# Kernel tuning notes

Measured on AMD Instinct MI355X. Metric: run time of the kernel, lower is better.

The kernel has to match this reference:

```python
import jax, jax.numpy as jnp
import numpy as np

G, NPG = 100, 500
N = G * NPG            # 50000 nodes, contiguous equal-size graphs
IN, H = 128, 256
L = 3                  # num_layers
K = 3                  # knn k (loop=True -> self included)
E = 16 * N             # 800000 edges

def setup_inputs():
    key = jax.random.key(0)
    k = jax.random.split(key, 8)
    x = jax.random.normal(k[0], (N, IN), jnp.float32)
    batch = jnp.repeat(jnp.arange(G, dtype=jnp.int32), NPG)
    gid = jax.random.randint(k[1], (E,), 0, G)
    src = jax.random.randint(k[2], (E,), 0, NPG) + gid * NPG
    dst = jax.random.randint(k[3], (E,), 0, NPG) + gid * NPG
    edge_index = jnp.stack([src, dst]).astype(jnp.int32)
    def lin(kk, fin, fout):
        return (jax.random.normal(kk, (fin, fout), jnp.float32) / np.sqrt(fin)).astype(jnp.float32)
    inp = dict(x=x, edge_index=edge_index, batch=batch)
    inp["emb_W"] = lin(k[4], IN, H); inp["emb_b"] = jnp.zeros((H,), jnp.float32)
    inp["conv_W"] = jnp.stack([lin(jax.random.fold_in(k[5], i), H, H) for i in range(L)])
    inp["conv_b"] = jnp.zeros((L, H), jnp.float32)
    inp["fconv_W"] = jnp.stack([lin(jax.random.fold_in(k[6], i), H, H) for i in range(L)])
    inp["fconv_b"] = jnp.zeros((L, H), jnp.float32)
    inp["norm_w"] = jnp.ones((L, H), jnp.float32); inp["norm_b"] = jnp.zeros((L, H), jnp.float32); inp["norm_ms"] = jnp.ones((L, H), jnp.float32)
    inp["fnorm_w"] = jnp.ones((L, H), jnp.float32); inp["fnorm_b"] = jnp.zeros((L, H), jnp.float32); inp["fnorm_ms"] = jnp.ones((L, H), jnp.float32)
    inp["gate_W"] = lin(k[7], 2 * H, H); inp["gate_b"] = jnp.zeros((H,), jnp.float32)
    return inp

def _gcn_conv(h, src, dst, W, b):
    # GCNConv: add self loops, symmetric deg^-1/2 normalization
    m = h @ W                                     # [N,H]
    loop = jnp.arange(N, dtype=src.dtype)
    s2 = jnp.concatenate([src, loop]); d2 = jnp.concatenate([dst, loop])
    deg = jax.ops.segment_sum(jnp.ones_like(d2, jnp.float32), d2, num_segments=N)
    dinv = jnp.where(deg > 0, jax.lax.rsqrt(deg), 0.0)
    coef = (dinv[s2] * dinv[d2])[:, None]
    return jax.ops.segment_sum(m[s2] * coef, d2, num_segments=N) + b

def _graph_norm(x, batch, w, b, ms, cnt):
    # PyG GraphNorm: out = w * (x - ms*mean) / sqrt(var + eps) + b, per-graph stats
    mean = jax.ops.segment_sum(x, batch, num_segments=G) / cnt
    out = x - mean[batch] * ms
    var = jax.ops.segment_sum(out * out, batch, num_segments=G) / cnt
    return w * out * jax.lax.rsqrt(var + 1e-5)[batch] + b

def _knn_graph(x):
    # per-graph cosine knn, loop=True (self has sim 1 and is kept)
    xr = x.reshape(G, NPG, -1)
    xn = xr / (jnp.linalg.norm(xr, axis=-1, keepdims=True) + 1e-12)
    sim = jnp.einsum('gnh,gmh->gnm', xn, xn)      # [G,NPG,NPG]
    _, idx = jax.lax.top_k(sim, K)                # [G,NPG,K]
    offs = (jnp.arange(G) * NPG)[:, None, None]
    src = (idx + offs).reshape(-1)
    dst = jnp.broadcast_to(jnp.arange(N).reshape(G, NPG, 1), (G, NPG, K)).reshape(-1)
    return src.astype(jnp.int32), dst.astype(jnp.int32)

def reference(x, edge_index, batch, emb_W, emb_b, conv_W, conv_b, norm_w, norm_b, norm_ms, fconv_W, fconv_b, fnorm_w, fnorm_b, fnorm_ms, gate_W, gate_b):
    cnt = jax.ops.segment_sum(jnp.ones((N,), jnp.float32), batch, num_segments=G)[:, None]
    h = x @ emb_W + emb_b
    fsrc, fdst = _knn_graph(h)
    src, dst = edge_index[0], edge_index[1]
    all_x = []
    for i in range(L - 1):   # eval mode: dropout is identity
        prev = h
        h = _gcn_conv(h, src, dst, conv_W[i], conv_b[i])
        h = jax.nn.leaky_relu(_graph_norm(h, batch, norm_w[i], norm_b[i], norm_ms[i], cnt))
        f = _gcn_conv(h, fsrc, fdst, fconv_W[i], fconv_b[i])
        f = jax.nn.leaky_relu(_graph_norm(f, batch, fnorm_w[i], fnorm_b[i], fnorm_ms[i], cnt))
        gate = jax.nn.sigmoid(jnp.concatenate([h, f], axis=-1) @ gate_W + gate_b)
        h = gate * h + (1.0 - gate) * f + prev
        all_x.append(h)
    # faithful to source: for i in range(L): += pool(all_x[i-1])  (Python negative indexing!)
    gf = jnp.zeros((G, H), jnp.float32)
    for i in range(L):
        gf = gf + jax.ops.segment_sum(all_x[i - 1], batch, num_segments=G) / cnt
    return gf
```

## Files before the change

### kernel.cpp

```cpp
#include <hip/hip_runtime.h>
#include <math.h>

#define NN 50000
#define GG 100
#define NPGc 500
#define HH 256
#define IND 128

typedef __attribute__((ext_vector_type(8))) short short8v;
typedef __attribute__((ext_vector_type(4))) float f32x4;

__device__ __forceinline__ ushort f2bf(float f) {
    union { float f; unsigned u; } v; v.f = f;
    unsigned r = (v.u + 0x7fffu + ((v.u >> 16) & 1u)) >> 16;
    return (ushort)r;
}
__device__ __forceinline__ float bf2f(ushort h) {
    union { unsigned u; float f; } v; v.u = ((unsigned)h) << 16;
    return v.f;
}

__device__ __forceinline__ int swz(int row, int kidx) { return kidx ^ ((row & 7) << 3); }

__global__ void wcvt_all(const float* __restrict__ emb_W, const float* __restrict__ conv_W,
                         const float* __restrict__ fconv_W, const float* __restrict__ gate_W,
                         ushort* __restrict__ dst)
{
    int i = blockIdx.x * 256 + threadIdx.x;
    if (i >= 425984) return;
    float v;
    if (i < 32768)       { int n = i >> 7, k = i & 127;              v = emb_W[(size_t)k * 256 + n]; }
    else if (i < 98304)  { int j = i - 32768;  int n = j >> 8, k = j & 255; v = conv_W[(size_t)k * 256 + n]; }
    else if (i < 163840) { int j = i - 98304;  int n = j >> 8, k = j & 255; v = conv_W[65536 + (size_t)k * 256 + n]; }
    else if (i < 229376) { int j = i - 163840; int n = j >> 8, k = j & 255; v = fconv_W[(size_t)k * 256 + n]; }
    else if (i < 294912) { int j = i - 229376; int n = j >> 8, k = j & 255; v = fconv_W[65536 + (size_t)k * 256 + n]; }
    else                 { int j = i - 294912; int n = j >> 9, k = j & 511; v = gate_W[(size_t)k * 256 + n]; }
    dst[i] = f2bf(v);
}

__global__ __launch_bounds__(256)
void gemm_mfma(const void* __restrict__ Av, const void* __restrict__ A2v, int abf,
               const ushort* __restrict__ Wt, const float* __restrict__ bias,
               float* __restrict__ C, ushort* __restrict__ Cbf,
               int M, int K, int lda, int mode,
               const ushort* __restrict__ hn, const ushort* __restrict__ fn,
               const void* __restrict__ prevv, int prevbf)
{
    __shared__ ushort As[128][64];
    __shared__ ushort Bs[128][64];
    const int bid = blockIdx.x;
    const int xcd = bid & 7;
    const int t = bid >> 3;
    const int cb = t & 1;
    const int rowblk = (t >> 1) * 8 + xcd;
    const int row0 = rowblk * 128;
    if (row0 >= M) return;
    const int col0 = cb * 128;
    const int tid = threadIdx.x;
    const int lane = tid & 63;
    const int w = tid >> 6;
    const int wr = (w >> 1) * 64, wc = (w & 1) * 64;
    const int lr = lane & 15, lk = (lane >> 4) * 8;
    f32x4 acc[4][4] = {};

    for (int k0 = 0; k0 < K; k0 += 64) {
        __syncthreads();
        #pragma unroll
        for (int it = 0; it < 4; ++it) {
            int c = it * 256 + tid;
            int row = c >> 3, col = (c & 7) * 8;
            int gr = row0 + row; if (gr > M - 1) gr = M - 1;
            int kk = k0 + col;
            if (abf) {
                const ushort* Ap = (const ushort*)Av;
                if (A2v != nullptr && kk >= 256) { Ap = (const ushort*)A2v; kk -= 256; }
                *(int4*)&As[row][swz(row, col)] =
                    *(const int4*)&Ap[(size_t)gr * lda + kk];
            } else {
                const float* Ap = (const float*)Av;
                if (A2v != nullptr && kk >= 256) { Ap = (const float*)A2v; kk -= 256; }
                const float* s = &Ap[(size_t)gr * lda + kk];
                float4 v0 = *(const float4*)s;
                float4 v1 = *(const float4*)(s + 4);
                union { ushort u[8]; int4 q; } pk;
                pk.u[0] = f2bf(v0.x); pk.u[1] = f2bf(v0.y); pk.u[2] = f2bf(v0.z); pk.u[3] = f2bf(v0.w);
                pk.u[4] = f2bf(v1.x); pk.u[5] = f2bf(v1.y); pk.u[6] = f2bf(v1.z); pk.u[7] = f2bf(v1.w);
                *(int4*)&As[row][swz(row, col)] = pk.q;
            }
        }
        #pragma unroll
        for (int it = 0; it < 4; ++it) {
            int c = it * 256 + tid;
            int n = c >> 3, k = (c & 7) * 8;
            *(int4*)&Bs[n][swz(n, k)] = *(const int4*)&Wt[(size_t)(col0 + n) * K + k0 + k];
        }
        __syncthreads();
        #pragma unroll
        for (int ks = 0; ks < 2; ++ks) {
            short8v av[4], bv[4];
            #pragma unroll
            for (int m = 0; m < 4; ++m) {
                int rr = wr + m * 16 + lr;
                av[m] = *(const short8v*)&As[rr][swz(rr, ks * 32 + lk)];
            }
            #pragma unroll
            for (int n = 0; n < 4; ++n) {
                int rr = wc + n * 16 + lr;
                bv[n] = *(const short8v*)&Bs[rr][swz(rr, ks * 32 + lk)];
            }
            #pragma unroll
            for (int m = 0; m < 4; ++m)
                #pragma unroll
                for (int n = 0; n < 4; ++n)
                    acc[m][n] = __builtin_amdgcn_mfma_f32_16x16x32_bf16(av[m], bv[n], acc[m][n], 0, 0, 0);
        }
    }
    const int fr = (lane >> 4) * 4;
    if (mode == 0) {
        #pragma unroll
        for (int n = 0; n < 4; ++n) {
            int col = col0 + wc + n * 16 + lr;
            float bb = bias ? bias[col] : 0.f;
            #pragma unroll
            for (int m = 0; m < 4; ++m) {
                int rbase = row0 + wr + m * 16 + fr;
                #pragma unroll
                for (int r = 0; r < 4; ++r) {
                    int row = rbase + r;
                    if (row < M) C[(size_t)row * HH + col] = acc[m][n][r] + bb;
                }
            }
        }
    } else if (mode == 2) {
        #pragma unroll
        for (int n = 0; n < 4; ++n) {
            int col = col0 + wc + n * 16 + lr;
            float bb = bias ? bias[col] : 0.f;
            #pragma unroll
            for (int m = 0; m < 4; ++m) {
                int rbase = row0 + wr + m * 16 + fr;
                #pragma unroll
                for (int r = 0; r < 4; ++r) {
                    int row = rbase + r;
                    if (row < M) Cbf[(size_t)row * HH + col] = f2bf(acc[m][n][r] + bb);
                }
            }
        }
    } else {
        #pragma unroll
        for (int n = 0; n < 4; ++n) {
            int col = col0 + wc + n * 16 + lr;
            float gb = bias[col];
            #pragma unroll
            for (int m = 0; m < 4; ++m) {
                int rbase = row0 + wr + m * 16 + fr;
                #pragma unroll
                for (int r = 0; r < 4; ++r) {
                    int row = rbase + r;
                    if (row < M) {
                        size_t o = (size_t)row * HH + col;
                        float z = acc[m][n][r] + gb;
                        float s = 1.f / (1.f + expf(-z));
                        float hv = bf2f(hn[o]);
                        float fv = bf2f(fn[o]);
                        float pv = prevbf ? bf2f(((const ushort*)prevv)[o])
                                          : ((const float*)prevv)[o];
                        Cbf[o] = f2bf(s * hv + (1.f - s) * fv + pv);
                    }
                }
            }
        }
    }
}

__global__ __launch_bounds__(256)
void row_norm_hl(const float* __restrict__ h, ushort* __restrict__ xh, ushort* __restrict__ xl)
{
    int n = blockIdx.x, c = threadIdx.x;
    float v = h[(size_t)n * HH + c];
    __shared__ float red[256];
    red[c] = v * v;
    __syncthreads();
    for (int s = 128; s > 0; s >>= 1) {
        if (c < s) red[c] += red[c + s];
        __syncthreads();
    }
    float norm = sqrtf(red[0]);
    float xn = v / (norm + 1e-12f);
    ushort hi = f2bf(xn);
    xh[(size_t)n * HH + c] = hi;
    xl[(size_t)n * HH + c] = f2bf(xn - bf2f(hi));
}

__device__ __forceinline__ bool tk_better(float va, int ia, float vb, int ib)
{
    return (va > vb) || (va == vb && ia < ib);
}

__device__ __forceinline__ void ins3(float v, int i,
                                     float& a0, int& b0, float& a1, int& b1,
                                     float& a2, int& b2)
{
    if (tk_better(v, i, a0, b0))      { a2 = a1; b2 = b1; a1 = a0; b1 = b0; a0 = v; b0 = i; }
    else if (tk_better(v, i, a1, b1)) { a2 = a1; b2 = b1; a1 = v;  b1 = i; }
    else if (tk_better(v, i, a2, b2)) { a2 = v;  b2 = i; }
}

__device__ __forceinline__ void merge3(float& v0, float& v1, float& v2,
                                       int& i0, int& i1, int& i2, int off)
{
    float w0 = __shfl_xor(v0, off), w1 = __shfl_xor(v1, off), w2 = __shfl_xor(v2, off);
    int   j0 = __shfl_xor(i0, off), j1 = __shfl_xor(i1, off), j2 = __shfl_xor(i2, off);
    float avv[3] = { v0, v1, v2 }, bvv[3] = { w0, w1, w2 };
    int   aii[3] = { i0, i1, i2 }, bii[3] = { j0, j1, j2 };
    float rv[3]; int ri[3];
    int p = 0, q = 0;
    #pragma unroll
    for (int t = 0; t < 3; ++t) {
        bool takeA = tk_better(avv[p], aii[p], bvv[q], bii[q]);
        rv[t] = takeA ? avv[p] : bvv[q];
        ri[t] = takeA ? aii[p] : bii[q];
        if (takeA) ++p; else ++q;
    }
    v0 = rv[0]; v1 = rv[1]; v2 = rv[2];
    i0 = ri[0]; i1 = ri[1]; i2 = ri[2];
}

__global__ __launch_bounds__(256, 1)
void simtopk(const ushort* __restrict__ xnh, const ushort* __restrict__ xnl,
             int* __restrict__ fsrc)
{
    __shared__ ushort Bs[2][2][128][36];
    const int bid = blockIdx.x;
    const int xcd = bid & 7;
    const int rb  = (bid >> 3) & 7;
    const int g   = (bid >> 6) * 8 + xcd;
    if (g >= GG) return;
    const int row0 = rb * 64;
    const int tid  = threadIdx.x;
    const int lane = tid & 63;
    const int w    = tid >> 6;
    const int lr   = lane & 15;
    const int hi4  = lane >> 4;
    const size_t base = (size_t)g * NPGc * HH;

    int arow = row0 + w * 16 + lr; if (arow > NPGc - 1) arow = NPGc - 1;
    const ushort* aph = xnh + base + (size_t)arow * HH + hi4 * 8;
    const ushort* apl = xnl + base + (size_t)arow * HH + hi4 * 8;
    short8v ah[8], al[8];
    #pragma unroll
    for (int kc = 0; kc < 8; ++kc) {
        ah[kc] = *(const short8v*)(aph + kc * 32);
        al[kc] = *(const short8v*)(apl + kc * 32);
    }

    const int scol = tid >> 1;
    const int sq   = (tid & 1) * 2;

    float tv0[4], tv1[4], tv2[4];
    int   ti0[4], ti1[4], ti2[4];
    #pragma unroll
    for (int r = 0; r < 4; ++r) {
        tv0[r] = tv1[r] = tv2[r] = -2.f;
        ti0[r] = ti1[r] = ti2[r] = 0x7fffffff;
    }

    for (int ct = 0; ct < 4; ++ct) {
        const int col0 = ct * 128;
        int gcol = col0 + scol; if (gcol > NPGc - 1) gcol = NPGc - 1;
        const ushort* sph = xnh + base + (size_t)gcol * HH + sq * 8;
        const ushort* spl = xnl + base + (size_t)gcol * HH + sq * 8;

        {
            int4 h0 = *(const int4*)(sph);
            int4 h1 = *(const int4*)(sph + 8);
            int4 l0 = *(const int4*)(spl);
            int4 l1 = *(const int4*)(spl + 8);
            *(int4*)&Bs[0][0][scol][sq * 8]     = h0;
            *(int4*)&Bs[0][0][scol][sq * 8 + 8] = h1;
            *(int4*)&Bs[0][1][scol][sq * 8]     = l0;
            *(int4*)&Bs[0][1][scol][sq * 8 + 8] = l1;
        }
        __syncthreads();

        f32x4 acc[8] = {};
        #pragma unroll
        for (int kc = 0; kc < 8; ++kc) {
            const int cur = kc & 1, nxt = cur ^ 1;
            int4 h0, h1, l0, l1;
            if (kc < 7) {
                const ushort* nh = sph + (kc + 1) * 32;
                const ushort* nl = spl + (kc + 1) * 32;
                h0 = *(const int4*)(nh);
                h1 = *(const int4*)(nh + 8);
                l0 = *(const int4*)(nl);
                l1 = *(const int4*)(nl + 8);
            }
            short8v bh[8], bl[8];
            #pragma unroll
            for (int n = 0; n < 8; ++n) {
                int rr = n * 16 + lr;
                bh[n] = *(const short8v*)&Bs[cur][0][rr][hi4 * 8];
                bl[n] = *(const short8v*)&Bs[cur][1][rr][hi4 * 8];
            }
            #pragma unroll
            for (int n = 0; n < 8; ++n) {
                acc[n] = __builtin_amdgcn_mfma_f32_16x16x32_bf16(ah[kc], bh[n], acc[n], 0, 0, 0);
                acc[n] = __builtin_amdgcn_mfma_f32_16x16x32_bf16(ah[kc], bl[n], acc[n], 0, 0, 0);
                acc[n] = __builtin_amdgcn_mfma_f32_16x16x32_bf16(al[kc], bh[n], acc[n], 0, 0, 0);
            }
            if (kc < 7) {
                *(int4*)&Bs[nxt][0][scol][sq * 8]     = h0;
                *(int4*)&Bs[nxt][0][scol][sq * 8 + 8] = h1;
                *(int4*)&Bs[nxt][1][scol][sq * 8]     = l0;
                *(int4*)&Bs[nxt][1][scol][sq * 8 + 8] = l1;
            }
            __syncthreads();
        }

        #pragma unroll
        for (int r = 0; r < 4; ++r) {
            float a0 = tv0[r], a1 = tv1[r], a2 = tv2[r];
            int   b0 = ti0[r], b1 = ti1[r], b2 = ti2[r];
            #pragma unroll
            for (int n = 0; n < 8; ++n) {
                int col = col0 + n * 16 + lr;
                if (col < NPGc)
                    ins3(acc[n][r], col, a0, b0, a1, b1, a2, b2);
            }
            tv0[r] = a0; tv1[r] = a1; tv2[r] = a2;
            ti0[r] = b0; ti1[r] = b1; ti2[r] = b2;
        }
    }

    #pragma unroll
    for (int r = 0; r < 4; ++r) {
        float a0 = tv0[r], a1 = tv1[r], a2 = tv2[r];
        int   b0 = ti0[r], b1 = ti1[r], b2 = ti2[r];
        #pragma unroll
        for (int off = 1; off <= 8; off <<= 1)
            merge3(a0, a1, a2, b0, b1, b2, off);
        if (lr == 0) {
            int row = row0 + w * 16 + hi4 * 4 + r;
            if (row < NPGc) {
                int rg = g * NPGc + row;
                fsrc[rg * 3 + 0] = g * NPGc + b0;
                fsrc[rg * 3 + 1] = g * NPGc + b1;
                fsrc[rg * 3 + 2] = g * NPGc + b2;
            }
        }
    }
}

__global__ void hist_kernel(const int* __restrict__ dst, int* __restrict__ cnt, int nE)
{
    int e = blockIdx.x * 256 + threadIdx.x;
    if (e < nE) atomicAdd(&cnt[dst[e]], 1);
}

__global__ void scan1_kernel(const int* __restrict__ in, int* __restrict__ out,
                             int* __restrict__ bsum, int n)
{
    __shared__ int sh[256];
    int t = threadIdx.x;
    int i = blockIdx.x * 256 + t;
    int v = (i < n) ? in[i] : 0;
    sh[t] = v;
    __syncthreads();
    for (int s = 1; s < 256; s <<= 1) {
        int tv = (t >= s) ? sh[t - s] : 0;
        __syncthreads();
        sh[t] += tv;
        __syncthreads();
    }
    if (i < n) out[i] = sh[t] - v;
    if (t == 255) bsum[blockIdx.x] = sh[255];
}

__global__ void scan2_kernel(int* __restrict__ bsum, int nb)
{
    __shared__ int sh[256];
    int t = threadIdx.x;
    int v = (t < nb) ? bsum[t] : 0;
    sh[t] = v;
    __syncthreads();
    for (int s = 1; s < 256; s <<= 1) {
        int tv = (t >= s) ? sh[t - s] : 0;
        __syncthreads();
        sh[t] += tv;
        __syncthreads();
    }
    if (t < nb) bsum[t] = sh[t] - v;
}

__global__ void scan3_kernel(int* __restrict__ out, const int* __restrict__ bsum, int n)
{
    int i = blockIdx.x * 256 + threadIdx.x;
    if (i < n) out[i] += bsum[blockIdx.x];
}

__global__ void fill_kernel(const int* __restrict__ src, const int* __restrict__ dst,
                            const int* __restrict__ row_ptr, int* __restrict__ cursor,
                            int* __restrict__ sorted_src, int nE)
{
    int e = blockIdx.x * 256 + threadIdx.x;
    if (e < nE) {
        int d = dst[e];
        int pos = row_ptr[d] + atomicAdd(&cursor[d], 1);
        sorted_src[pos] = src[e];
    }
}

__global__ void dinv_kernel(const int* __restrict__ cnt, float* __restrict__ dinv, int n)
{
    int i = blockIdx.x * 256 + threadIdx.x;
    if (i < n) dinv[i] = rsqrtf((float)cnt[i] + 1.0f);
}

__global__ __launch_bounds__(256)
void gcn_gather(const ushort* __restrict__ m, const int* __restrict__ row_ptr,
                const int* __restrict__ cnt, const int* __restrict__ srcs,
                const float* __restrict__ dinv, const float* __restrict__ bias,
                ushort* __restrict__ out)
{
    int bid = blockIdx.x;
    int xcd = bid & 7, idx = bid >> 3;
    int g = xcd + 8 * (idx / NPGc);
    if (g >= GG) return;
    int n = g * NPGc + (idx % NPGc);
    int c = threadIdx.x;
    float dn = dinv[n];
    float acc = bf2f(m[(size_t)n * HH + c]) * dn;
    int s0 = row_ptr[n], e0 = s0 + cnt[n];
    for (int e = s0; e < e0; ++e) {
        int s = srcs[e];
        acc += bf2f(m[(size_t)s * HH + c]) * dinv[s];
    }
    out[(size_t)n * HH + c] = f2bf(acc * dn + bias[c]);
}

__global__ __launch_bounds__(256)
void fgcn_gather(const ushort* __restrict__ m, const int* __restrict__ fsrc,
                 const float* __restrict__ bias, ushort* __restrict__ out)
{
    int bid = blockIdx.x;
    int xcd = bid & 7, idx = bid >> 3;
    int g = xcd + 8 * (idx / NPGc);
    if (g >= GG) return;
    int n = g * NPGc + (idx % NPGc);
    int c = threadIdx.x;
    int s0 = fsrc[n * 3], s1 = fsrc[n * 3 + 1], s2 = fsrc[n * 3 + 2];
    float acc = bf2f(m[(size_t)n * HH + c]) + bf2f(m[(size_t)s0 * HH + c])
              + bf2f(m[(size_t)s1 * HH + c]) + bf2f(m[(size_t)s2 * HH + c]);
    out[(size_t)n * HH + c] = f2bf(0.25f * acc + bias[c]);
}

__global__ __launch_bounds__(256)
void norm_stats(const ushort* __restrict__ x, float* __restrict__ S1p, float* __restrict__ S2p)
{
    int g = blockIdx.x, chunk = blockIdx.y, c = threadIdx.x;
    int r0 = chunk * 63, r1 = min(r0 + 63, NPGc);
    float s1 = 0.f, s2 = 0.f;
    for (int r = r0; r < r1; ++r) {
        float v = bf2f(x[((size_t)(g * NPGc + r)) * HH + c]);
        s1 += v; s2 += v * v;
    }
    size_t o = ((size_t)(g * 8 + chunk)) * HH + c;
    S1p[o] = s1;
    S2p[o] = s2;
}

__global__ __launch_bounds__(256)
void norm_reduce(const float* __restrict__ S1p, const float* __restrict__ S2p,
                 const float* __restrict__ ms, float* __restrict__ MM, float* __restrict__ RS)
{
    int g = blockIdx.x, c = threadIdx.x;
    float s1 = 0.f, s2 = 0.f;
    #pragma unroll
    for (int j = 0; j < 8; ++j) {
        size_t po = ((size_t)(g * 8 + j)) * HH + c;
        s1 += S1p[po];
        s2 += S2p[po];
    }
    float mean = s1 / (float)NPGc;
    float mm = mean * ms[c];
    float var = s2 / (float)NPGc - 2.f * mm * mean + mm * mm;
    MM[g * HH + c] = mm;
    RS[g * HH + c] = rsqrtf(var + 1e-5f);
}

__global__ __launch_bounds__(256)
void norm_apply(ushort* __restrict__ x, const float* __restrict__ MM, const float* __restrict__ RS,
                const float* __restrict__ w, const float* __restrict__ b)
{
    int n = blockIdx.x, c = threadIdx.x;
    int g = n / NPGc;
    size_t o = (size_t)n * HH + c;
    float v = bf2f(x[o]);
    float outv = w[c] * (v - MM[g * HH + c]) * RS[g * HH + c] + b[c];
    x[o] = f2bf(outv > 0.f ? outv : 0.01f * outv);
}

__global__ __launch_bounds__(256)
void pool_kernel(const ushort* __restrict__ X0, const ushort* __restrict__ X1,
                 float* __restrict__ out)
{
    int g = blockIdx.x, c = threadIdx.x;
    float s0 = 0.f, s1 = 0.f;
    for (int r = 0; r < NPGc; ++r) {
        size_t o = ((size_t)(g * NPGc + r)) * HH + c;
        s0 += bf2f(X0[o]);
        s1 += bf2f(X1[o]);
    }
    out[g * HH + c] = (s0 + 2.f * s1) / (float)NPGc;
}

__global__ void sentinel_kernel(float* out, int n)
{
    int i = blockIdx.x * 256 + threadIdx.x;
    if (i < n) out[i] = 12345.0f;
}

extern "C" void kernel_launch(void* const* d_in, const int* in_sizes, int n_in,
                              void* d_out, int out_size, void* d_ws, size_t ws_size,
                              hipStream_t stream)
{
    const float* x       = (const float*)d_in[0];
    const int* edge_idx  = (const int*)d_in[1];
    const float* emb_W   = (const float*)d_in[3];
    const float* emb_b   = (const float*)d_in[4];
    const float* conv_W  = (const float*)d_in[5];
    const float* conv_b  = (const float*)d_in[6];
    const float* fconv_W = (const float*)d_in[7];
    const float* fconv_b = (const float*)d_in[8];
    const float* norm_w  = (const float*)d_in[9];
    const float* norm_b  = (const float*)d_in[10];
    const float* norm_ms = (const float*)d_in[11];
    const float* fnorm_w = (const float*)d_in[12];
    const float* fnorm_b = (const float*)d_in[13];
    const float* fnorm_ms= (const float*)d_in[14];
    const float* gate_W  = (const float*)d_in[15];
    const float* gate_b  = (const float*)d_in[16];

    const int E = in_sizes[1] / 2;
    const int* esrc = edge_idx;
    const int* edst = edge_idx + E;

    const size_t NHf = (size_t)NN * HH;
    char* p = (char*)d_ws;
    auto alloc = [&](size_t bytes) { char* r = p; p += (bytes + 255) & ~(size_t)255; return r; };
    float*  B0 = (float*)alloc(NHf * 4);
    ushort* Mr = (ushort*)alloc(NHf * 2);
    ushort* Ar = (ushort*)alloc(NHf * 2);
    ushort* Br = (ushort*)alloc(NHf * 2);
    ushort* H0 = (ushort*)alloc(NHf * 2);
    ushort* H1 = (ushort*)alloc(NHf * 2);
    ushort* xnh = Mr;
    ushort* xnl = Ar;
    int* sorted_src = (int*)alloc((size_t)E * 4);
    int* row_ptr    = (int*)alloc((size_t)NN * 4);
    int* deg_cnt    = (int*)alloc((size_t)NN * 4);
    int* cursor     = (int*)alloc((size_t)NN * 4);
    float* dinv     = (float*)alloc((size_t)NN * 4);
    int* fsrc       = (int*)alloc((size_t)NN * 3 * 4);
    float* S1p      = (float*)alloc((size_t)GG * 8 * HH * 4);
    float* S2p      = (float*)alloc((size_t)GG * 8 * HH * 4);
    float* MM       = (float*)alloc((size_t)GG * HH * 4);
    float* RS       = (float*)alloc((size_t)GG * HH * 4);
    int* bsum       = (int*)alloc(1024);
    ushort* wts     = (ushort*)alloc((size_t)425984 * 2);
    size_t needed = (size_t)(p - (char*)d_ws);
    if (ws_size < needed) {
        sentinel_kernel<<<(out_size + 255) / 256, 256, 0, stream>>>((float*)d_out, out_size);
        return;
    }
    ushort* embWt   = wts;
    ushort* convWt0 = wts + 32768;
    ushort* convWt1 = wts + 98304;
    ushort* fconvWt0 = wts + 163840;
    ushort* fconvWt1 = wts + 229376;
    ushort* gateWt  = wts + 294912;

    const int nScanB = (NN + 255) / 256;
    const int gatherGrid = 8 * 13 * NPGc;
    const int gemmGrid = 8 * 49 * 2;

    hipMemsetAsync(deg_cnt, 0, (size_t)NN * 4, stream);
    hipMemsetAsync(cursor, 0, (size_t)NN * 4, stream);

    wcvt_all<<<1664, 256, 0, stream>>>(emb_W, conv_W, fconv_W, gate_W, wts);

    gemm_mfma<<<gemmGrid, 256, 0, stream>>>(x, nullptr, 0, embWt, emb_b, B0, nullptr,
                                            NN, IND, IND, 0, nullptr, nullptr, nullptr, 0);

    hist_kernel<<<(E + 255) / 256, 256, 0, stream>>>(edst, deg_cnt, E);
    scan1_kernel<<<nScanB, 256, 0, stream>>>(deg_cnt, row_ptr, bsum, NN);
    scan2_kernel<<<1, 256, 0, stream>>>(bsum, nScanB);
    scan3_kernel<<<nScanB, 256, 0, stream>>>(row_ptr, bsum, NN);
    fill_kernel<<<(E + 255) / 256, 256, 0, stream>>>(esrc, edst, row_ptr, cursor, sorted_src, E);
    dinv_kernel<<<(NN + 255) / 256, 256, 0, stream>>>(deg_cnt, dinv, NN);

    row_norm_hl<<<NN, 256, 0, stream>>>(B0, xnh, xnl);
    simtopk<<<832, 256, 0, stream>>>(xnh, xnl, fsrc);

    dim3 ngrid(GG, 8);
    const void* hptr = (const void*)B0;
    int habf = 0;
    ushort* Hout[2] = { H0, H1 };
    for (int i = 0; i < 2; ++i) {
        const ushort* Wc = (i == 0) ? convWt0 : convWt1;
        const ushort* Wf = (i == 0) ? fconvWt0 : fconvWt1;
        const float* bc  = conv_b  + (size_t)i * HH;
        const float* bf  = fconv_b + (size_t)i * HH;
        gemm_mfma<<<gemmGrid, 256, 0, stream>>>(hptr, nullptr, habf, Wc, nullptr, nullptr, Mr,
                                                NN, HH, HH, 2, nullptr, nullptr, nullptr, 0);
        gcn_gather<<<gatherGrid, 256, 0, stream>>>(Mr, row_ptr, deg_cnt, sorted_src,
                                                   dinv, bc, Ar);
        norm_stats<<<ngrid, 256, 0, stream>>>(Ar, S1p, S2p);
        norm_reduce<<<GG, 256, 0, stream>>>(S1p, S2p, norm_ms + i * HH, MM, RS);
        norm_apply<<<NN, 256, 0, stream>>>(Ar, MM, RS, norm_w + i * HH, norm_b + i * HH);
        gemm_mfma<<<gemmGrid, 256, 0, stream>>>(Ar, nullptr, 1, Wf, nullptr, nullptr, Mr,
                                                NN, HH, HH, 2, nullptr, nullptr, nullptr, 0);
        fgcn_gather<<<gatherGrid, 256, 0, stream>>>(Mr, fsrc, bf, Br);
        norm_stats<<<ngrid, 256, 0, stream>>>(Br, S1p, S2p);
        norm_reduce<<<GG, 256, 0, stream>>>(S1p, S2p, fnorm_ms + i * HH, MM, RS);
        norm_apply<<<NN, 256, 0, stream>>>(Br, MM, RS, fnorm_w + i * HH, fnorm_b + i * HH);
        gemm_mfma<<<gemmGrid, 256, 0, stream>>>(Ar, Br, 1, gateWt, gate_b, nullptr, Hout[i],
                                                NN, 2 * HH, HH, 1, Ar, Br, hptr, habf);
        hptr = (const void*)Hout[i];
        habf = 1;
    }
    pool_kernel<<<GG, 256, 0, stream>>>(H0, H1, (float*)d_out);
}
```

Before: 1.264 ms.

## Fuse GraphNorm apply and leaky-ReLU into GEMM operand loads and gate epilogue

Removes the standalone norm_apply kernels. The GraphNorm affine plus leaky-ReLU is now applied on the fly when loading bf16 A tiles into shared memory, and again in the gate GEMM epilogue for the h and f values. This saves two full read-write passes over the N×256 activations per layer and two launches. In exchange, the normalization is recomputed redundantly: once per column block in the A load and again in the epilogue. Each A load also performs extra per-graph statistic loads.

```diff
diff --git a/kernel.cpp b/kernel.cpp
--- a/kernel.cpp
+++ b/kernel.cpp
@@ -19,6 +19,7 @@
     union { unsigned u; float f; } v; v.u = ((unsigned)h) << 16;
     return v.f;
 }
+__device__ __forceinline__ float lrelu(float v) { return v > 0.f ? v : 0.01f * v; }
 
 __device__ __forceinline__ int swz(int row, int kidx) { return kidx ^ ((row & 7) << 3); }
 
@@ -43,8 +44,11 @@
                const ushort* __restrict__ Wt, const float* __restrict__ bias,
                float* __restrict__ C, ushort* __restrict__ Cbf,
                int M, int K, int lda, int mode,
-               const ushort* __restrict__ hn, const ushort* __restrict__ fn,
-               const void* __restrict__ prevv, int prevbf)
+               const void* __restrict__ prevv, int prevbf,
+               const float* __restrict__ MMa, const float* __restrict__ RSa,
+               const float* __restrict__ nwa, const float* __restrict__ nba,
+               const float* __restrict__ MMb, const float* __restrict__ RSb,
+               const float* __restrict__ nwb, const float* __restrict__ nbb)
 {
     __shared__ ushort As[128][64];
     __shared__ ushort Bs[128][64];
@@ -73,9 +77,37 @@
             int kk = k0 + col;
             if (abf) {
                 const ushort* Ap = (const ushort*)Av;
-                if (A2v != nullptr && kk >= 256) { Ap = (const ushort*)A2v; kk -= 256; }
-                *(int4*)&As[row][swz(row, col)] =
-                    *(const int4*)&Ap[(size_t)gr * lda + kk];
+                const float *MMp = MMa, *RSp = RSa, *wp = nwa, *bp = nba;
+                if (A2v != nullptr && kk >= 256) {
+                    Ap = (const ushort*)A2v; kk -= 256;
+                    MMp = MMb; RSp = RSb; wp = nwb; bp = nbb;
+                }
+                int4 raw = *(const int4*)&Ap[(size_t)gr * lda + kk];
+                if (MMp != nullptr) {
+                    int g = gr / NPGc;
+                    const ushort* rp = (const ushort*)&raw;
+                    float4 mm0 = *(const float4*)&MMp[(size_t)g * HH + kk];
+                    float4 mm1 = *(const float4*)&MMp[(size_t)g * HH + kk + 4];
+                    float4 rs0 = *(const float4*)&RSp[(size_t)g * HH + kk];
+                    float4 rs1 = *(const float4*)&RSp[(size_t)g * HH + kk + 4];
+                    float4 w0 = *(const float4*)&wp[kk];
+                    float4 w1 = *(const float4*)&wp[kk + 4];
+                    float4 b0 = *(const float4*)&bp[kk];
+                    float4 b1 = *(const float4*)&bp[kk + 4];
+                    float mms[8] = { mm0.x, mm0.y, mm0.z, mm0.w, mm1.x, mm1.y, mm1.z, mm1.w };
+                    float rss[8] = { rs0.x, rs0.y, rs0.z, rs0.w, rs1.x, rs1.y, rs1.z, rs1.w };
+                    float wss[8] = { w0.x, w0.y, w0.z, w0.w, w1.x, w1.y, w1.z, w1.w };
+                    float bss[8] = { b0.x, b0.y, b0.z, b0.w, b1.x, b1.y, b1.z, b1.w };
+                    union { ushort u[8]; int4 q; } pk;
+                    #pragma unroll
+                    for (int j = 0; j < 8; ++j) {
+                        float v = bf2f(rp[j]);
+                        pk.u[j] = f2bf(lrelu(wss[j] * (v - mms[j]) * rss[j] + bss[j]));
+                    }
+                    *(int4*)&As[row][swz(row, col)] = pk.q;
+                } else {
+                    *(int4*)&As[row][swz(row, col)] = raw;
+                }
             } else {
                 const float* Ap = (const float*)Av;
                 if (A2v != nullptr && kk >= 256) { Ap = (const float*)A2v; kk -= 256; }
@@ -147,10 +179,14 @@
             }
         }
     } else {
+        const ushort* hraw = (const ushort*)Av;
+        const ushort* fraw = (const ushort*)A2v;
         #pragma unroll
         for (int n = 0; n < 4; ++n) {
             int col = col0 + wc + n * 16 + lr;
             float gb = bias[col];
+            float wh = nwa[col], bh = nba[col];
+            float wf = nwb[col], bf2 = nbb[col];
             #pragma unroll
             for (int m = 0; m < 4; ++m) {
                 int rbase = row0 + wr + m * 16 + fr;
@@ -159,10 +195,12 @@
                     int row = rbase + r;
                     if (row < M) {
                         size_t o = (size_t)row * HH + col;
+                        int g = row / NPGc;
+                        size_t go = (size_t)g * HH + col;
                         float z = acc[m][n][r] + gb;
                         float s = 1.f / (1.f + expf(-z));
-                        float hv = bf2f(hn[o]);
-                        float fv = bf2f(fn[o]);
+                        float hv = lrelu(wh * (bf2f(hraw[o]) - MMa[go]) * RSa[go] + bh);
+                        float fv = lrelu(wf * (bf2f(fraw[o]) - MMb[go]) * RSb[go] + bf2);
                         float pv = prevbf ? bf2f(((const ushort*)prevv)[o])
                                           : ((const float*)prevv)[o];
                         Cbf[o] = f2bf(s * hv + (1.f - s) * fv + pv);
@@ -487,18 +525,6 @@
     float var = s2 / (float)NPGc - 2.f * mm * mean + mm * mm;
     MM[g * HH + c] = mm;
     RS[g * HH + c] = rsqrtf(var + 1e-5f);
-}
-
-__global__ __launch_bounds__(256)
-void norm_apply(ushort* __restrict__ x, const float* __restrict__ MM, const float* __restrict__ RS,
-                const float* __restrict__ w, const float* __restrict__ b)
-{
-    int n = blockIdx.x, c = threadIdx.x;
-    int g = n / NPGc;
-    size_t o = (size_t)n * HH + c;
-    float v = bf2f(x[o]);
-    float outv = w[c] * (v - MM[g * HH + c]) * RS[g * HH + c] + b[c];
-    x[o] = f2bf(outv > 0.f ? outv : 0.01f * outv);
 }
 
 __global__ __launch_bounds__(256)
@@ -565,8 +591,10 @@
     int* fsrc       = (int*)alloc((size_t)NN * 3 * 4);
     float* S1p      = (float*)alloc((size_t)GG * 8 * HH * 4);
     float* S2p      = (float*)alloc((size_t)GG * 8 * HH * 4);
-    float* MM       = (float*)alloc((size_t)GG * HH * 4);
-    float* RS       = (float*)alloc((size_t)GG * HH * 4);
+    float* MMh      = (float*)alloc((size_t)GG * HH * 4);
+    float* RSh      = (float*)alloc((size_t)GG * HH * 4);
+    float* MMf      = (float*)alloc((size_t)GG * HH * 4);
+    float* RSf      = (float*)alloc((size_t)GG * HH * 4);
     int* bsum       = (int*)alloc(1024);
     ushort* wts     = (ushort*)alloc((size_t)425984 * 2);
     size_t needed = (size_t)(p - (char*)d_ws);
@@ -591,7 +619,9 @@
     wcvt_all<<<1664, 256, 0, stream>>>(emb_W, conv_W, fconv_W, gate_W, wts);
 
     gemm_mfma<<<gemmGrid, 256, 0, stream>>>(x, nullptr, 0, embWt, emb_b, B0, nullptr,
-                                            NN, IND, IND, 0, nullptr, nullptr, nullptr, 0);
+                                            NN, IND, IND, 0, nullptr, 0,
+                                            nullptr, nullptr, nullptr, nullptr,
+                                            nullptr, nullptr, nullptr, nullptr);
 
     hist_kernel<<<(E + 255) / 256, 256, 0, stream>>>(edst, deg_cnt, E);
     scan1_kernel<<<nScanB, 256, 0, stream>>>(deg_cnt, row_ptr, bsum, NN);
@@ -611,22 +641,32 @@
         const ushort* Wc = (i == 0) ? convWt0 : convWt1;
         const ushort* Wf = (i == 0) ? fconvWt0 : fconvWt1;
         const float* bc  = conv_b  + (size_t)i * HH;
-        const float* bf  = fconv_b + (size_t)i * HH;
+        const float* bfb = fconv_b + (size_t)i * HH;
+        const float* nw  = norm_w  + (size_t)i * HH;
+        const float* nb  = norm_b  + (size_t)i * HH;
+        const float* nms = norm_ms + (size_t)i * HH;
+        const float* fw  = fnorm_w + (size_t)i * HH;
+        const float* fb  = fnorm_b + (size_t)i * HH;
+        const float* fms = fnorm_ms+ (size_t)i * HH;
         gemm_mfma<<<gemmGrid, 256, 0, stream>>>(hptr, nullptr, habf, Wc, nullptr, nullptr, Mr,
-                                                NN, HH, HH, 2, nullptr, nullptr, nullptr, 0);
+                                                NN, HH, HH, 2, nullptr, 0,
+                                                nullptr, nullptr, nullptr, nullptr,
+                                                nullptr, nullptr, nullptr, nullptr);
         gcn_gather<<<gatherGrid, 256, 0, stream>>>(Mr, row_ptr, deg_cnt, sorted_src,
                                                    dinv, bc, Ar);
         norm_stats<<<ngrid, 256, 0, stream>>>(Ar, S1p, S2p);
-        norm_reduce<<<GG, 256, 0, stream>>>(S1p, S2p, norm_ms + i * HH, MM, RS);
-        norm_apply<<<NN, 256, 0, stream>>>(Ar, MM, RS, norm_w + i * HH, norm_b + i * HH);
+        norm_reduce<<<GG, 256, 0, stream>>>(S1p, S2p, nms, MMh, RSh);
         gemm_mfma<<<gemmGrid, 256, 0, stream>>>(Ar, nullptr, 1, Wf, nullptr, nullptr, Mr,
-                                                NN, HH, HH, 2, nullptr, nullptr, nullptr, 0);
-        fgcn_gather<<<gatherGrid, 256, 0, stream>>>(Mr, fsrc, bf, Br);
+                                                NN, HH, HH, 2, nullptr, 0,
+                                                MMh, RSh, nw, nb,
+                                                nullptr, nullptr, nullptr, nullptr);
+        fgcn_gather<<<gatherGrid, 256, 0, stream>>>(Mr, fsrc, bfb, Br);
         norm_stats<<<ngrid, 256, 0, stream>>>(Br, S1p, S2p);
-        norm_reduce<<<GG, 256, 0, stream>>>(S1p, S2p, fnorm_ms + i * HH, MM, RS);
-        norm_apply<<<NN, 256, 0, stream>>>(Br, MM, RS, fnorm_w + i * HH, fnorm_b + i * HH);
+        norm_reduce<<<GG, 256, 0, stream>>>(S1p, S2p, fms, MMf, RSf);
         gemm_mfma<<<gemmGrid, 256, 0, stream>>>(Ar, Br, 1, gateWt, gate_b, nullptr, Hout[i],
-                                                NN, 2 * HH, HH, 1, Ar, Br, hptr, habf);
+                                                NN, 2 * HH, HH, 1, hptr, habf,
+                                                MMh, RSh, nw, nb,
+                                                MMf, RSf, fw, fb);
         hptr = (const void*)Hout[i];
         habf = 1;
     }
```

After: 1.249 ms. Within noise of the previous version (-1.2%).
